# Kernel optimization log

Measured on AMD Instinct MI355X. Metric: run time of the kernel, lower is better.

The kernel has to match this reference:

```python
import jax, jax.numpy as jnp
import numpy as np

NUM_HEADS = 16
HEAD_DIM = 64  # hidden_size 1024 / 16 heads


def setup_inputs() -> dict:
    key = jax.random.key(0)
    ks = jax.random.split(key, 4)
    B, S, H = 2, 2048, 1024
    scale = 1.0 / np.sqrt(H)
    return {
        "hidden_states": jax.random.normal(ks[0], (B, S, H), dtype=jnp.float32),
        "attention_mask": jnp.zeros((B, 1, 1, S), dtype=jnp.float32),
        "Wq": jax.random.normal(ks[1], (H, H), dtype=jnp.float32) * scale,
        "bq": jnp.zeros((H,), dtype=jnp.float32),
        "Wk": jax.random.normal(ks[2], (H, H), dtype=jnp.float32) * scale,
        "bk": jnp.zeros((H,), dtype=jnp.float32),
        "Wv": jax.random.normal(ks[3], (H, H), dtype=jnp.float32) * scale,
        "bv": jnp.zeros((H,), dtype=jnp.float32),
    }


def reference(hidden_states, attention_mask, Wq, bq, Wk, bk, Wv, bv):
    B, S, H = hidden_states.shape
    h, d = NUM_HEADS, HEAD_DIM

    def heads(x):  # [B,S,H] -> [B,h,S,d]
        return x.reshape(B, S, h, d).transpose(0, 2, 1, 3)

    q = heads(hidden_states @ Wq + bq)
    k = heads(hidden_states @ Wk + bk)
    v = heads(hidden_states @ Wv + bv)

    # [B,h,S,S] scores, scaled then additive-masked (HF BERT semantics)
    scores = jnp.einsum("bhqd,bhkd->bhqk", q, k) / jnp.sqrt(jnp.float32(d))
    scores = scores + attention_mask
    probs = jax.nn.softmax(scores, axis=-1)  # dropout p=0 -> identity

    ctx = jnp.einsum("bhqk,bhkd->bhqd", probs, v)
    ctx = ctx.transpose(0, 2, 1, 3).reshape(B, S, H)
    return ctx
```

## Files before the change

### kernel.cpp

```cpp
#include <hip/hip_runtime.h>
#include <hip/hip_bf16.h>


#define SEQ   2048
#define HID   1024
#define NHEAD 16
#define HD    64
#define SD    ((size_t)SEQ * HD)

typedef __bf16 bf16x8 __attribute__((ext_vector_type(8)));
typedef float  f32x4  __attribute__((ext_vector_type(4)));

#define L2E 1.4426950408889634f
#define SOFT_OFF 16.0f

__device__ __forceinline__ unsigned short f2b(float f) {
    unsigned int x = __float_as_uint(f);
    x += 0x7FFFu + ((x >> 16) & 1u);
    return (unsigned short)(x >> 16);
}

__device__ __forceinline__ void gload16(const unsigned short* g,
                                        unsigned short* l) {
    __builtin_amdgcn_global_load_lds(
        (const __attribute__((address_space(1))) unsigned int*)g,
        (__attribute__((address_space(3))) unsigned int*)l, 16, 0, 0);
}

__global__ __launch_bounds__(256) void cvt_x_k(const float* __restrict__ X,
                                               unsigned short* __restrict__ Xb)
{
    const size_t i = ((size_t)blockIdx.x * 256 + threadIdx.x) * 4;
    const float4 v = *(const float4*)(X + i);
    ushort4 o;
    o.x = f2b(v.x); o.y = f2b(v.y); o.z = f2b(v.z); o.w = f2b(v.w);
    *(ushort4*)(Xb + i) = o;
}

__global__ __launch_bounds__(256) void cvt_w_k(
    const float* __restrict__ Wq, const float* __restrict__ Wk,
    const float* __restrict__ Wv, unsigned short* __restrict__ Wtb)
{
    __shared__ __align__(16) unsigned short T[64][68];
    const int z = blockIdx.z;
    const float* __restrict__ W = (z == 0) ? Wq : (z == 1) ? Wk : Wv;
    const int k0 = blockIdx.x * 64, n0 = blockIdx.y * 64;
    const int tid = threadIdx.x;
    #pragma unroll
    for (int it = 0; it < 16; ++it) {
        const int idx = 256 * it + tid;
        const int r = idx >> 6, c = idx & 63;
        T[c][r] = f2b(W[(size_t)(k0 + r) * HID + n0 + c]);
    }
    __syncthreads();
    unsigned short* dst = Wtb + (size_t)z * HID * HID;
    #pragma unroll
    for (int it = 0; it < 4; ++it) {
        const int idx = 256 * it + tid;
        const int n = idx >> 4, c4 = (idx & 15) * 4;
        *(ushort4*)(dst + (size_t)(n0 + n) * HID + k0 + c4) = *(ushort4*)&T[n][c4];
    }
}

__global__ __launch_bounds__(512) void qkv_gemm_fused(
    const unsigned short* __restrict__ Xb, const unsigned short* __restrict__ Wtb,
    const float* __restrict__ bq, const float* __restrict__ bk,
    const float* __restrict__ bv, unsigned short* __restrict__ scratch)
{
    __shared__ __align__(16) unsigned char pool[65536];
    unsigned short (*Xs)[128][32] = (unsigned short (*)[128][32])pool;
    unsigned short (*Ws)[3][128][32] = (unsigned short (*)[3][128][32])(pool + 16384);

    const int tid = threadIdx.x, w = tid >> 6, lane = tid & 63;
    const int ln = lane & 15, quad = lane >> 4;
    const int wr = (w >> 2) * 64;
    const int wc = (w & 3) * 32;
    const int m0 = blockIdx.x * 128, n0 = blockIdx.y * 128;

    const int rS = w * 16 + (lane >> 2);
    const int cS = (lane & 3) * 8;

    f32x4 acc[3][4][2];
    #pragma unroll
    for (int z = 0; z < 3; ++z)
        #pragma unroll
        for (int i = 0; i < 4; ++i)
            #pragma unroll
            for (int j = 0; j < 2; ++j) acc[z][i][j] = (f32x4){0.f, 0.f, 0.f, 0.f};

    {
        unsigned short* lx = &Xs[0][0][0] + (size_t)w * 512;
        gload16(Xb + (size_t)(m0 + rS) * HID + cS, lx);
        #pragma unroll
        for (int z = 0; z < 3; ++z) {
            unsigned short* lw = &Ws[0][z][0][0] + (size_t)w * 512;
            gload16(Wtb + (size_t)z * HID * HID + (size_t)(n0 + rS) * HID + cS, lw);
        }
    }

    int cur = 0;
    for (int k0 = 0; k0 < HID; k0 += 32) {
        __syncthreads();
        if (k0 + 32 < HID) {
            const int kn = k0 + 32, nxt = cur ^ 1;
            unsigned short* lx = &Xs[nxt][0][0] + (size_t)w * 512;
            gload16(Xb + (size_t)(m0 + rS) * HID + kn + cS, lx);
            #pragma unroll
            for (int z = 0; z < 3; ++z) {
                unsigned short* lw = &Ws[nxt][z][0][0] + (size_t)w * 512;
                gload16(Wtb + (size_t)z * HID * HID + (size_t)(n0 + rS) * HID + kn + cS, lw);
            }
        }

        bf16x8 am[4];
        #pragma unroll
        for (int t = 0; t < 4; ++t)
            am[t] = *(const bf16x8*)&Xs[cur][wr + t * 16 + ln][quad * 8];
        #pragma unroll
        for (int z = 0; z < 3; ++z) {
            bf16x8 bn[2];
            #pragma unroll
            for (int n = 0; n < 2; ++n)
                bn[n] = *(const bf16x8*)&Ws[cur][z][wc + n * 16 + ln][quad * 8];
            #pragma unroll
            for (int mt = 0; mt < 4; ++mt)
                #pragma unroll
                for (int nt = 0; nt < 2; ++nt)
                    acc[z][mt][nt] = __builtin_amdgcn_mfma_f32_16x16x32_bf16(
                        am[mt], bn[nt], acc[z][mt][nt], 0, 0, 0);
        }
        cur ^= 1;
    }

    __syncthreads();
    const int b = m0 >> 11;
    const int srow0 = (m0 + wr) & (SEQ - 1);
    const int head = (n0 + wc) >> 6;
    const int dimb = (n0 + wc) & 63;

    unsigned short (*EtQ)[36] = (unsigned short (*)[36])(pool + (size_t)w * 4352);
    #pragma unroll
    for (int z = 0; z < 2; ++z) {
        const float* __restrict__ Bp = (z == 0) ? bq : bk;
        float bias[2];
        #pragma unroll
        for (int nt = 0; nt < 2; ++nt) bias[nt] = Bp[n0 + wc + nt * 16 + ln];
        #pragma unroll
        for (int half = 0; half < 2; ++half) {
            #pragma unroll
            for (int mt2 = 0; mt2 < 2; ++mt2) {
                const int mt = half * 2 + mt2;
                #pragma unroll
                for (int nt = 0; nt < 2; ++nt)
                    #pragma unroll
                    for (int r = 0; r < 4; ++r)
                        EtQ[mt2 * 16 + quad * 4 + r][nt * 16 + ln] =
                            f2b(acc[z][mt][nt][r] + bias[nt]);
            }
            #pragma unroll
            for (int it = 0; it < 4; ++it) {
                const int row = it * 8 + (lane >> 3), c4 = (lane & 7) * 4;
                *(ushort4*)(scratch +
                    ((size_t)(z * 32 + b * NHEAD + head) * SEQ + srow0
                     + half * 32 + row) * HD + dimb + c4) =
                    *(const ushort4*)&EtQ[row][c4];
            }
        }
    }
    {
        unsigned short (*EtV)[68] = (unsigned short (*)[68])(pool + (size_t)w * 4352);
        float bias[2];
        #pragma unroll
        for (int nt = 0; nt < 2; ++nt) bias[nt] = bv[n0 + wc + nt * 16 + ln];
        #pragma unroll
        for (int nt = 0; nt < 2; ++nt)
            #pragma unroll
            for (int mt = 0; mt < 4; ++mt) {
                ushort4 o;
                o.x = f2b(acc[2][mt][nt][0] + bias[nt]);
                o.y = f2b(acc[2][mt][nt][1] + bias[nt]);
                o.z = f2b(acc[2][mt][nt][2] + bias[nt]);
                o.w = f2b(acc[2][mt][nt][3] + bias[nt]);
                *(ushort4*)&EtV[nt * 16 + ln][mt * 16 + quad * 4] = o;
            }
        #pragma unroll
        for (int it = 0; it < 8; ++it) {
            const int d = it * 4 + quad, s4 = ln * 4;
            *(ushort4*)(scratch +
                ((size_t)(64 + b * NHEAD + head) * HD + dimb + d) * SEQ
                + srow0 + s4) = *(const ushort4*)&EtV[d][s4];
        }
    }
}

__device__ __forceinline__ void gemm_epilogue(
    f32x4 acc[4][4], const float* __restrict__ Bp,
    unsigned short* __restrict__ scratch, unsigned short (*Et)[68],
    int z, int m0, int n0, int wr, int wc, int ln, int quad)
{
    const int b = m0 >> 11;
    const int srow0 = (m0 + wr) & (SEQ - 1);
    const int head = (n0 + wc) >> 6;
    __syncthreads();

    if (z == 2) {
        #pragma unroll
        for (int half = 0; half < 2; ++half) {
            #pragma unroll
            for (int nt2 = 0; nt2 < 2; ++nt2) {
                const int nt = half * 2 + nt2;
                const float bias = Bp[n0 + wc + nt * 16 + ln];
                #pragma unroll
                for (int mt = 0; mt < 4; ++mt) {
                    ushort4 o;
                    o.x = f2b(acc[mt][nt][0] + bias);
                    o.y = f2b(acc[mt][nt][1] + bias);
                    o.z = f2b(acc[mt][nt][2] + bias);
                    o.w = f2b(acc[mt][nt][3] + bias);
                    *(ushort4*)&Et[nt2 * 16 + ln][mt * 16 + quad * 4] = o;
                }
            }
            __syncthreads();
            #pragma unroll
            for (int it = 0; it < 8; ++it) {
                const int d = it * 4 + quad, s4 = ln * 4;
                *(ushort4*)(scratch +
                    ((size_t)(64 + b * NHEAD + head) * HD + half * 32 + d) * SEQ
                    + srow0 + s4) = *(const ushort4*)&Et[d][s4];
            }
            __syncthreads();
        }
    } else {
        #pragma unroll
        for (int half = 0; half < 2; ++half) {
            #pragma unroll
            for (int mt2 = 0; mt2 < 2; ++mt2) {
                const int mt = half * 2 + mt2;
                #pragma unroll
                for (int nt = 0; nt < 4; ++nt) {
                    const float bias = Bp[n0 + wc + nt * 16 + ln];
                    #pragma unroll
                    for (int r = 0; r < 4; ++r)
                        Et[mt2 * 16 + quad * 4 + r][nt * 16 + ln] =
                            f2b(acc[mt][nt][r] + bias);
                }
            }
            __syncthreads();
            #pragma unroll
            for (int it = 0; it < 8; ++it) {
                const int r = it * 4 + quad, c4 = ln * 4;
                *(ushort4*)(scratch +
                    ((size_t)(z * 32 + b * NHEAD + head) * SEQ + srow0
                     + half * 32 + r) * HD + c4) = *(const ushort4*)&Et[r][c4];
            }
            __syncthreads();
        }
    }
}

__global__ __launch_bounds__(256) void qkv_gemm_fp32(
    const float* __restrict__ X,
    const float* __restrict__ Wq, const float* __restrict__ bq,
    const float* __restrict__ Wk, const float* __restrict__ bk,
    const float* __restrict__ Wv, const float* __restrict__ bv,
    unsigned short* __restrict__ scratch)
{
    __shared__ __align__(16) unsigned char pool[20480];
    unsigned short (*Xs)[40] = (unsigned short (*)[40])pool;
    unsigned short (*Wt)[40] = (unsigned short (*)[40])(pool + 10240);

    const int z = blockIdx.z;
    const float* __restrict__ W  = (z == 0) ? Wq : (z == 1) ? Wk : Wv;
    const float* __restrict__ Bp = (z == 0) ? bq : (z == 1) ? bk : bv;

    const int tid = threadIdx.x, w = tid >> 6, lane = tid & 63;
    const int ln = lane & 15, quad = lane >> 4;
    const int wr = (w >> 1) * 64, wc = (w & 1) * 64;
    const int m0 = blockIdx.x * 128, n0 = blockIdx.y * 128;

    const int xr = tid >> 3, xc = (tid & 7) * 4;
    const int wkr = tid >> 5, wnc = (tid & 31) * 4;

    f32x4 acc[4][4];
    #pragma unroll
    for (int i = 0; i < 4; ++i)
        #pragma unroll
        for (int j = 0; j < 4; ++j) acc[i][j] = (f32x4){0.f, 0.f, 0.f, 0.f};

    for (int k0 = 0; k0 < HID; k0 += 32) {
        __syncthreads();
        #pragma unroll
        for (int it = 0; it < 4; ++it) {
            const int r = xr + 32 * it;
            const float4 xv = *(const float4*)(X + (size_t)(m0 + r) * HID + k0 + xc);
            ushort4 xb;
            xb.x = f2b(xv.x); xb.y = f2b(xv.y); xb.z = f2b(xv.z); xb.w = f2b(xv.w);
            *(ushort4*)&Xs[r][xc] = xb;
            const int kr = wkr + 8 * it;
            const float4 wv = *(const float4*)(W + (size_t)(k0 + kr) * HID + n0 + wnc);
            Wt[wnc + 0][kr] = f2b(wv.x);
            Wt[wnc + 1][kr] = f2b(wv.y);
            Wt[wnc + 2][kr] = f2b(wv.z);
            Wt[wnc + 3][kr] = f2b(wv.w);
        }
        __syncthreads();
        bf16x8 am[4], bn[4];
        #pragma unroll
        for (int t = 0; t < 4; ++t) {
            am[t] = *(const bf16x8*)&Xs[wr + t * 16 + ln][quad * 8];
            bn[t] = *(const bf16x8*)&Wt[wc + t * 16 + ln][quad * 8];
        }
        #pragma unroll
        for (int mt = 0; mt < 4; ++mt)
            #pragma unroll
            for (int nt = 0; nt < 4; ++nt)
                acc[mt][nt] = __builtin_amdgcn_mfma_f32_16x16x32_bf16(
                    am[mt], bn[nt], acc[mt][nt], 0, 0, 0);
    }
    unsigned short (*Et)[68] = (unsigned short (*)[68])(pool + (size_t)w * 4352);
    gemm_epilogue(acc, Bp, scratch, Et, z, m0, n0, wr, wc, ln, quad);
}

__global__ __launch_bounds__(256) void attn_mfma(
    const unsigned short* __restrict__ scratch,
    const float* __restrict__ mask,
    float* __restrict__ out)
{
    __shared__ __align__(16) unsigned char smem[37888];
    unsigned short (*Ks)[64][72] = (unsigned short (*)[64][72])smem;
    unsigned short (*Vt)[64][72] = (unsigned short (*)[64][72])(smem + 18432);
    float* lrbuf = (float*)(smem + 36864);
    float (*OA)[68] = (float (*)[68])smem;
    float (*OB)[68] = (float (*)[68])(smem + 18432);

    const int orig = blockIdx.x;
    const int wg = ((orig & 7) << 7) + (orig >> 3);
    const int qt = wg & 31;
    const int bh = wg >> 5;
    const int b = bh >> 4, head = bh & 15;

    const unsigned short* __restrict__ Qp  = scratch + (size_t)bh * SD;
    const unsigned short* __restrict__ Kp  = scratch + (size_t)(32 + bh) * SD;
    const unsigned short* __restrict__ Vtp = scratch + (size_t)(64 + bh) * SD;
    const float* __restrict__ maskp = mask + b * SEQ;

    const int tid = threadIdx.x, w = tid >> 6, lane = tid & 63;
    const int ln = lane & 15, quad = lane >> 4;
    const int wk0 = w * 16;

    bf16x8 qb[4][2];
    #pragma unroll
    for (int t = 0; t < 4; ++t)
        #pragma unroll
        for (int h = 0; h < 2; ++h)
            qb[t][h] = *(const bf16x8*)(Qp +
                (size_t)(qt * 64 + t * 16 + ln) * HD + h * 32 + quad * 8);

    f32x4 O[4][4];
    #pragma unroll
    for (int i = 0; i < 4; ++i)
        #pragma unroll
        for (int j = 0; j < 4; ++j) O[i][j] = (f32x4){0.f, 0.f, 0.f, 0.f};
    float lr[4] = {0.f, 0.f, 0.f, 0.f};

    const int sr8 = tid >> 3, sc8 = (tid & 7) * 8;

    {
        uint4 a = *(const uint4*)(Kp + (size_t)sr8 * HD + sc8);
        uint4 c = *(const uint4*)(Kp + (size_t)(sr8 + 32) * HD + sc8);
        uint4 d = *(const uint4*)(Vtp + (size_t)sr8 * SEQ + sc8);
        uint4 e = *(const uint4*)(Vtp + (size_t)(sr8 + 32) * SEQ + sc8);
        *(uint4*)&Ks[0][sr8][sc8]      = a;
        *(uint4*)&Ks[0][sr8 + 32][sc8] = c;
        *(uint4*)&Vt[0][sr8][sc8]      = d;
        *(uint4*)&Vt[0][sr8 + 32][sc8] = e;
    }
    uint4 kg0 = *(const uint4*)(Kp + (size_t)(64 + sr8) * HD + sc8);
    uint4 kg1 = *(const uint4*)(Kp + (size_t)(64 + sr8 + 32) * HD + sc8);
    uint4 vg0 = *(const uint4*)(Vtp + (size_t)sr8 * SEQ + 64 + sc8);
    uint4 vg1 = *(const uint4*)(Vtp + (size_t)(sr8 + 32) * SEQ + 64 + sc8);
    __syncthreads();

    const float cc = 0.125f * L2E;

    for (int kt = 0; kt < 32; ++kt) {
        const int cur = kt & 1;
        if (kt < 31) {
            *(uint4*)&Ks[cur ^ 1][sr8][sc8]      = kg0;
            *(uint4*)&Ks[cur ^ 1][sr8 + 32][sc8] = kg1;
            *(uint4*)&Vt[cur ^ 1][sr8][sc8]      = vg0;
            *(uint4*)&Vt[cur ^ 1][sr8 + 32][sc8] = vg1;
        }
        if (kt < 30) {
            const int kn = kt + 2;
            kg0 = *(const uint4*)(Kp + (size_t)(kn * 64 + sr8) * HD + sc8);
            kg1 = *(const uint4*)(Kp + (size_t)(kn * 64 + sr8 + 32) * HD + sc8);
            vg0 = *(const uint4*)(Vtp + (size_t)sr8 * SEQ + kn * 64 + sc8);
            vg1 = *(const uint4*)(Vtp + (size_t)(sr8 + 32) * SEQ + kn * 64 + sc8);
        }

        const bf16x8 ka0 = *(const bf16x8*)&Ks[cur][wk0 + ln][quad * 8];
        const bf16x8 ka1 = *(const bf16x8*)&Ks[cur][wk0 + ln][32 + quad * 8];

        uint2 vl[4];
        #pragma unroll
        for (int dg = 0; dg < 4; ++dg)
            vl[dg] = *(const uint2*)&Vt[cur][dg * 16 + ln][wk0 + quad * 4];

        f32x4 s[4];
        #pragma unroll
        for (int t = 0; t < 4; ++t) {
            f32x4 a = (f32x4){0.f, 0.f, 0.f, 0.f};
            a = __builtin_amdgcn_mfma_f32_16x16x32_bf16(ka0, qb[t][0], a, 0, 0, 0);
            a = __builtin_amdgcn_mfma_f32_16x16x32_bf16(ka1, qb[t][1], a, 0, 0, 0);
            s[t] = a;
        }

        const float4 mk4 = *(const float4*)(maskp + kt * 64 + wk0 + quad * 4);
        const float b0 = fmaf(mk4.x, L2E, -SOFT_OFF);
        const float b1 = fmaf(mk4.y, L2E, -SOFT_OFF);
        const float b2 = fmaf(mk4.z, L2E, -SOFT_OFF);
        const float b3 = fmaf(mk4.w, L2E, -SOFT_OFF);

        bf16x8 pb[4];
        #pragma unroll
        for (int t = 0; t < 4; ++t) {
            const float p0 = exp2f(fmaf(s[t][0], cc, b0));
            const float p1 = exp2f(fmaf(s[t][1], cc, b1));
            const float p2 = exp2f(fmaf(s[t][2], cc, b2));
            const float p3 = exp2f(fmaf(s[t][3], cc, b3));
            lr[t] += (p0 + p1) + (p2 + p3);
            unsigned int w0, w1;
            asm("v_cvt_pk_bf16_f32 %0, %1, %2" : "=v"(w0) : "v"(p0), "v"(p1));
            asm("v_cvt_pk_bf16_f32 %0, %1, %2" : "=v"(w1) : "v"(p2), "v"(p3));
            uint4 pu; pu.x = w0; pu.y = w1; pu.z = w0; pu.w = w1;
            pb[t] = *(bf16x8*)&pu;
        }

        #pragma unroll
        for (int dg = 0; dg < 4; ++dg) {
            uint4 vu; vu.x = vl[dg].x; vu.y = vl[dg].y; vu.z = 0u; vu.w = 0u;
            const bf16x8 va = *(bf16x8*)&vu;
            #pragma unroll
            for (int t = 0; t < 4; ++t)
                O[dg][t] = __builtin_amdgcn_mfma_f32_16x16x32_bf16(
                    va, pb[t], O[dg][t], 0, 0, 0);
        }

        __syncthreads();
    }

    #pragma unroll
    for (int t = 0; t < 4; ++t) {
        lr[t] += __shfl_xor(lr[t], 16);
        lr[t] += __shfl_xor(lr[t], 32);
    }
    if (quad == 0) {
        #pragma unroll
        for (int t = 0; t < 4; ++t) lrbuf[w * 64 + t * 16 + ln] = lr[t];
    }

    #define O_WRITE(BUF) { \
        _Pragma("unroll") for (int dg = 0; dg < 4; ++dg) \
        _Pragma("unroll") for (int t = 0; t < 4; ++t) \
            *(float4*)&BUF[t * 16 + ln][dg * 16 + quad * 4] = \
                *(float4*)&O[dg][t]; }
    #define O_ADD(BUF) { \
        _Pragma("unroll") for (int dg = 0; dg < 4; ++dg) \
        _Pragma("unroll") for (int t = 0; t < 4; ++t) { \
            const float4 x = *(const float4*)&BUF[t * 16 + ln][dg * 16 + quad * 4]; \
            O[dg][t][0] += x.x; O[dg][t][1] += x.y; \
            O[dg][t][2] += x.z; O[dg][t][3] += x.w; } }

    if (w == 1) O_WRITE(OA);
    if (w == 3) O_WRITE(OB);
    __syncthreads();
    if (w == 0) O_ADD(OA);
    if (w == 2) O_ADD(OB);
    __syncthreads();
    if (w == 2) O_WRITE(OA);
    __syncthreads();
    if (w == 0) { O_ADD(OA); O_WRITE(OA); }
    __syncthreads();

    #pragma unroll
    for (int it = 0; it < 4; ++it) {
        const int r = (tid >> 4) + 16 * it, c4 = (tid & 15) * 4;
        const float lrt = lrbuf[r] + lrbuf[64 + r] + lrbuf[128 + r] + lrbuf[192 + r];
        const float inv = 1.0f / lrt;
        float4 v = *(const float4*)&OA[r][c4];
        v.x *= inv; v.y *= inv; v.z *= inv; v.w *= inv;
        *(float4*)(out + ((size_t)b * SEQ + qt * 64 + r) * HID + head * HD + c4) = v;
    }
    #undef O_WRITE
    #undef O_ADD
}

extern "C" void kernel_launch(void* const* d_in, const int* in_sizes, int n_in,
                              void* d_out, int out_size, void* d_ws, size_t ws_size,
                              hipStream_t stream) {
    const float* X    = (const float*)d_in[0];
    const float* mask = (const float*)d_in[1];
    const float* Wq   = (const float*)d_in[2];
    const float* bq   = (const float*)d_in[3];
    const float* Wk   = (const float*)d_in[4];
    const float* bk   = (const float*)d_in[5];
    const float* Wv   = (const float*)d_in[6];
    const float* bv   = (const float*)d_in[7];

    unsigned short* scratch = (unsigned short*)d_ws;
    float* out = (float*)d_out;

    const bool big = (ws_size >= (40ull << 20));
    if (big) {
        unsigned short* Xb  = scratch + 96 * SD;
        unsigned short* Wtb = Xb + (size_t)2 * SEQ * HID;
        cvt_x_k<<<4096, 256, 0, stream>>>(X, Xb);
        cvt_w_k<<<dim3(16, 16, 3), 256, 0, stream>>>(Wq, Wk, Wv, Wtb);
        qkv_gemm_fused<<<dim3(32, 8), 512, 0, stream>>>(
            Xb, Wtb, bq, bk, bv, scratch);
    } else {
        qkv_gemm_fp32<<<dim3(32, 8, 3), 256, 0, stream>>>(
            X, Wq, bq, Wk, bk, Wv, bv, scratch);
    }
    attn_mfma<<<1024, 256, 0, stream>>>(scratch, mask, out);
}
```

Baseline: 196.0 us.

## Halve QKV GEMM N-tile to 64 and remap blocks for XCD locality

The fused QKV GEMM now uses 256-thread blocks with a 128x64 output tile, down from 512 threads and 128x128. It launches 512 blocks instead of 256, so the 256 CUs are better filled and LDS per block shrinks. The linear block index is permuted so consecutive blocks that land on the same XCD share N columns, which should help L2 reuse of weights. The staging load mapping is rewritten for the new tile shape. In exchange, the X tile is reloaded twice as often across blocks, and the epilogue (not shown) must still be consistent with the new wr/wc layout.

```diff
diff --git a/kernel.cpp b/kernel.cpp
--- a/kernel.cpp
+++ b/kernel.cpp
@@ -62,23 +62,23 @@
     }
 }
 
-__global__ __launch_bounds__(512) void qkv_gemm_fused(
+__global__ __launch_bounds__(256) void qkv_gemm_fused(
     const unsigned short* __restrict__ Xb, const unsigned short* __restrict__ Wtb,
     const float* __restrict__ bq, const float* __restrict__ bk,
     const float* __restrict__ bv, unsigned short* __restrict__ scratch)
 {
-    __shared__ __align__(16) unsigned char pool[65536];
+    __shared__ __align__(16) unsigned char pool[40960];
     unsigned short (*Xs)[128][32] = (unsigned short (*)[128][32])pool;
-    unsigned short (*Ws)[3][128][32] = (unsigned short (*)[3][128][32])(pool + 16384);
+    unsigned short (*Ws)[3][64][32] = (unsigned short (*)[3][64][32])(pool + 16384);
+
+    const int orig = blockIdx.x;
+    const int wg = ((orig & 7) << 6) + (orig >> 3);
+    const int m0 = (wg & 31) * 128, n0 = (wg >> 5) * 64;
 
     const int tid = threadIdx.x, w = tid >> 6, lane = tid & 63;
     const int ln = lane & 15, quad = lane >> 4;
-    const int wr = (w >> 2) * 64;
-    const int wc = (w & 3) * 32;
-    const int m0 = blockIdx.x * 128, n0 = blockIdx.y * 128;
-
-    const int rS = w * 16 + (lane >> 2);
-    const int cS = (lane & 3) * 8;
+    const int wr = (w >> 1) * 64;
+    const int wc = (w & 1) * 32;
 
     f32x4 acc[3][4][2];
     #pragma unroll
@@ -88,28 +88,27 @@
             #pragma unroll
             for (int j = 0; j < 2; ++j) acc[z][i][j] = (f32x4){0.f, 0.f, 0.f, 0.f};
 
-    {
-        unsigned short* lx = &Xs[0][0][0] + (size_t)w * 512;
-        gload16(Xb + (size_t)(m0 + rS) * HID + cS, lx);
-        #pragma unroll
-        for (int z = 0; z < 3; ++z) {
-            unsigned short* lw = &Ws[0][z][0][0] + (size_t)w * 512;
-            gload16(Wtb + (size_t)z * HID * HID + (size_t)(n0 + rS) * HID + cS, lw);
-        }
-    }
+    #define STAGE(BUF, K0) { \
+        _Pragma("unroll") for (int j = 0; j < 2; ++j) { \
+            const int L = w * 128 + j * 64 + lane; \
+            unsigned short* l = &Xs[BUF][0][0] + (size_t)(w * 128 + j * 64) * 8; \
+            gload16(Xb + (size_t)(m0 + (L >> 2)) * HID + (K0) + (L & 3) * 8, l); \
+        } \
+        _Pragma("unroll") for (int j = 0; j < 3; ++j) { \
+            const int L = w * 192 + j * 64 + lane; \
+            const int z_ = L >> 8, r_ = (L & 255) >> 2, c_ = (L & 3) * 8; \
+            unsigned short* l = &Ws[BUF][0][0][0] + (size_t)(w * 192 + j * 64) * 8; \
+            gload16(Wtb + (size_t)z_ * HID * HID + (size_t)(n0 + r_) * HID + (K0) + c_, l); \
+        } }
+
+    STAGE(0, 0);
 
     int cur = 0;
     for (int k0 = 0; k0 < HID; k0 += 32) {
         __syncthreads();
         if (k0 + 32 < HID) {
-            const int kn = k0 + 32, nxt = cur ^ 1;
-            unsigned short* lx = &Xs[nxt][0][0] + (size_t)w * 512;
-            gload16(Xb + (size_t)(m0 + rS) * HID + kn + cS, lx);
-            #pragma unroll
-            for (int z = 0; z < 3; ++z) {
-                unsigned short* lw = &Ws[nxt][z][0][0] + (size_t)w * 512;
-                gload16(Wtb + (size_t)z * HID * HID + (size_t)(n0 + rS) * HID + kn + cS, lw);
-            }
+            const int nxt = cur ^ 1;
+            STAGE(nxt, k0 + 32);
         }
 
         bf16x8 am[4];
@@ -131,6 +130,7 @@
         }
         cur ^= 1;
     }
+    #undef STAGE
 
     __syncthreads();
     const int b = m0 >> 11;
@@ -517,7 +517,7 @@
         unsigned short* Wtb = Xb + (size_t)2 * SEQ * HID;
         cvt_x_k<<<4096, 256, 0, stream>>>(X, Xb);
         cvt_w_k<<<dim3(16, 16, 3), 256, 0, stream>>>(Wq, Wk, Wv, Wtb);
-        qkv_gemm_fused<<<dim3(32, 8), 512, 0, stream>>>(
+        qkv_gemm_fused<<<512, 256, 0, stream>>>(
             Xb, Wtb, bq, bk, bv, scratch);
     } else {
         qkv_gemm_fp32<<<dim3(32, 8, 3), 256, 0, stream>>>(
```

Result: no change. 195.1 us (-0.5%).
